# Optimization experiments

Measured on AMD Instinct MI355X. Metric: run time of the kernel, lower is better.

The kernel has to match this reference:

```python
import jax, jax.numpy as jnp
import numpy as np

B, S, F, H = 256, 512, 64, 128
ODE_STEPS = 4
MAX_DT = 1.0


def setup_inputs() -> dict:
    key = jax.random.key(0)
    ks = jax.random.split(key, 11)
    D = F + H  # concat(x_t, h) width
    xav = float(np.sqrt(6.0 / (D + H)))          # xavier_uniform for gate weights
    bsc = float(1.0 / np.sqrt(D))                # torch Linear default bias init
    x = jax.random.normal(ks[0], (B, S, F), jnp.float32)
    time_diffs = jax.random.uniform(ks[1], (B, S), jnp.float32, 0.1, 2.0)
    def w(k):
        return jax.random.uniform(k, (D, H), jnp.float32, -xav, xav)
    def b(k):
        return jax.random.uniform(k, (H,), jnp.float32, -bsc, bsc)
    return {
        "x": x, "time_diffs": time_diffs,
        "W_i": w(ks[2]), "b_i": b(ks[3]),
        "W_f": w(ks[4]), "b_f": b(ks[5]),
        "W_o": w(ks[6]), "b_o": b(ks[7]),
        "W_g": w(ks[8]), "b_g": b(ks[9]),
    }


def reference(x, time_diffs, W_i, b_i, W_f, b_f, W_o, b_o, W_g, b_g):
    def ode_func(x_t, h, c):
        comb = jnp.concatenate([x_t, h], axis=-1)  # [B, F+H]
        i = jax.nn.sigmoid(comb @ W_i + b_i)
        f = jax.nn.sigmoid(comb @ W_f + b_f)
        o = jax.nn.sigmoid(comb @ W_o + b_o)
        g = jnp.tanh(comb @ W_g + b_g)
        dc = i * g + f * c - c
        dh = o * jnp.tanh(c) - h
        return dh, dc

    def rk4_step(x_t, h, c, dt):  # dt: [B, 1]
        k1h, k1c = ode_func(x_t, h, c)
        k2h, k2c = ode_func(x_t, h + 0.5 * dt * k1h, c + 0.5 * dt * k1c)
        k3h, k3c = ode_func(x_t, h + 0.5 * dt * k2h, c + 0.5 * dt * k2c)
        k4h, k4c = ode_func(x_t, h + dt * k3h, c + dt * k3c)
        h_new = h + dt / 6.0 * (k1h + 2 * k2h + 2 * k3h + k4h)
        c_new = c + dt / 6.0 * (k1c + 2 * k2c + 2 * k3c + k4c)
        return h_new, c_new

    def time_step(carry, inp):
        h, c = carry
        x_t, dtv = inp  # x_t [B,F], dtv [B]
        sub_dt = (jnp.minimum(dtv, MAX_DT) / ODE_STEPS)[:, None]  # [B,1]
        def body(hc, _):
            hh, cc = hc
            return rk4_step(x_t, hh, cc, sub_dt), None
        (h, c), _ = jax.lax.scan(body, (h, c), None, length=ODE_STEPS)
        return (h, c), h

    h0 = jnp.zeros((x.shape[0], H), x.dtype)
    c0 = jnp.zeros((x.shape[0], H), x.dtype)
    xs = (jnp.swapaxes(x, 0, 1), jnp.swapaxes(time_diffs, 0, 1))  # [S,B,F], [S,B]
    _, hs = jax.lax.scan(time_step, (h0, c0), xs)  # [S,B,H]
    return jnp.swapaxes(hs, 0, 1)  # [B,S,H]
```

## Files before the change

kernel.cpp:

```cpp
#include <hip/hip_runtime.h>


#define B_N 256
#define S_N 512
#define F_N 64
#define H_N 128

typedef _Float16 v8h __attribute__((ext_vector_type(8)));
typedef float v4f __attribute__((ext_vector_type(4)));

#define PIN_V(x) asm("" : "+v"(x))
#define MFMA16(a, b, c) __builtin_amdgcn_mfma_f32_16x16x32_f16((a), (b), (c), 0, 0, 0)
#define SB0() __builtin_amdgcn_sched_barrier(0)
#define BAR() do { SB0(); \
                   asm volatile("s_waitcnt lgkmcnt(0)" ::: "memory"); \
                   __builtin_amdgcn_s_barrier(); SB0(); } while (0)

static __device__ __forceinline__ float sigm(float x) {
  float e = __builtin_amdgcn_exp2f(-1.442695040888963f * x);
  return __builtin_amdgcn_rcpf(1.0f + e);
}

__global__ void __launch_bounds__(512, 2) clstm_mfma6(
    const float* __restrict__ x,
    const float* __restrict__ td,
    const float* __restrict__ Wi, const float* __restrict__ bi,
    const float* __restrict__ Wf, const float* __restrict__ bff,
    const float* __restrict__ Wo, const float* __restrict__ bo,
    const float* __restrict__ Wg, const float* __restrict__ bg,
    float* __restrict__ out)
{
  const int b    = blockIdx.x;
  const int t    = threadIdx.x;
  const int wv   = t >> 6;
  const int l    = t & 63;
  const int col  = l & 15;
  const int quad = l >> 4;
  const int n    = wv * 16 + col;

  const float* Wptr[4] = {Wi, Wf, Wo, Wg};

  v8h Bh[4][4];
  v8h Bx[4][2];
#pragma unroll
  for (int g = 0; g < 4; ++g) {
    const float* W = Wptr[g];
#pragma unroll
    for (int kt = 0; kt < 4; ++kt) {
      v8h f;
#pragma unroll
      for (int j = 0; j < 8; ++j)
        f[j] = (_Float16)W[(64 + kt * 32 + quad * 8 + j) * H_N + n];
      Bh[g][kt] = f;
      PIN_V(Bh[g][kt]);
    }
#pragma unroll
    for (int kt = 0; kt < 2; ++kt) {
      v8h f;
#pragma unroll
      for (int j = 0; j < 8; ++j)
        f[j] = (_Float16)W[(kt * 32 + quad * 8 + j) * H_N + n];
      Bx[g][kt] = f;
      PIN_V(Bx[g][kt]);
    }
  }
  float bias[4];
#pragma unroll
  for (int g = 0; g < 4; ++g)
    bias[g] = (g == 0 ? bi : g == 1 ? bff : g == 2 ? bo : bg)[n];

  __shared__ alignas(16) _Float16 lds_h[2][H_N];
  __shared__ alignas(16) _Float16 lds_x[F_N];
  __shared__ float lds_td[S_N];

  lds_td[t] = td[b * S_N + t];
  if (t < 32) {
    const float* xr = x + (size_t)b * S_N * F_N;
    lds_x[2 * t]     = (_Float16)xr[2 * t];
    lds_x[2 * t + 1] = (_Float16)xr[2 * t + 1];
  }
  if (t < H_N) lds_h[0][t] = (_Float16)0.0f;

  float h0v = 0.f, c0v = 0.f;
  float h_ev = 0.f, c_ev = 0.f;
  float sum_h = 0.f, sum_c = 0.f;
  float dt = 0.f, hdt = 0.f, d6 = 0.f, d6p = 0.f;
  const v4f zf = {0.f, 0.f, 0.f, 0.f};
  v4f ci2 = zf, ci3 = zf, cf2 = zf, cf3 = zf, cg2 = zf, cg3 = zf;
  v4f xpD[4] = {zf, zf, zf, zf};
  float xn0 = 0.f, xn1 = 0.f;

  for (int s = 0; s < S_N; ++s) {
#pragma unroll
    for (int ode = 0; ode < 4; ++ode) {
#pragma unroll
      for (int st = 0; st < 4; ++st) {
        BAR();
        const _Float16* hb = lds_h[st & 1];
        v8h ah0 = *(const v8h*)(hb + quad * 8);
        v8h ah1 = *(const v8h*)(hb + 32 + quad * 8);
        v8h ah2 = *(const v8h*)(hb + 64 + quad * 8);
        v8h ah3 = *(const v8h*)(hb + 96 + quad * 8);

        if (ode == 0 && st == 0) {
          dt  = fminf(lds_td[s], 1.0f) * 0.25f;
          hdt = 0.5f * dt;
          d6  = dt * (1.0f / 6.0f);
          v8h ax0 = *(const v8h*)(lds_x + quad * 8);
          v8h ax1 = *(const v8h*)(lds_x + 32 + quad * 8);
#pragma unroll
          for (int g = 0; g < 4; ++g) {
            float bv = bias[g];
            v4f cbv = {bv, bv, bv, bv};
            v4f a = MFMA16(ax0, Bx[g][0], cbv);
            xpD[g] = MFMA16(ax1, Bx[g][1], a);
          }
          xn0 = 0.f; xn1 = 0.f;
          if (t < 32 && s + 1 < S_N) {
            const float* xr = x + (size_t)(b * S_N + s + 1) * F_N;
            xn0 = xr[2 * t]; xn1 = xr[2 * t + 1];
          }
        }
        SB0();

        float tc;
        {
          const int pr = (st == 0) ? 3 : st - 1;
          float pi = ci2[0] + ci3[0];
          float pf = cf2[0] + cf3[0];
          float pg = cg2[0] + cg3[0];
          float ai = sigm(pi);
          float af = sigm(pf);
          float ag = fmaf(2.0f, sigm(2.0f * pg), -1.0f);
          float kc = fmaf(ai, ag, (af - 1.0f) * c_ev);
          float cnx;
          if (pr == 0)      { sum_c = kc;                      cnx = fmaf(hdt, kc, c0v); }
          else if (pr == 1) { sum_c = fmaf(2.f, kc, sum_c);    cnx = fmaf(hdt, kc, c0v); }
          else if (pr == 2) { sum_c = fmaf(2.f, kc, sum_c);    cnx = fmaf(dt, kc, c0v); }
          else {
            float sc = sum_c + kc;
            float dd = (ode == 0 && st == 0) ? d6p : d6;
            c0v = fmaf(dd, sc, c0v);
            cnx = c0v;
          }
          c_ev = cnx;
          tc = fmaf(2.0f, sigm(2.0f * c_ev), -1.0f);
        }
        SB0();

        v4f co2 = MFMA16(ah0, Bh[2][0], xpD[2]);
        co2     = MFMA16(ah1, Bh[2][1], co2);
        v4f co3 = MFMA16(ah2, Bh[2][2], zf);
        co3     = MFMA16(ah3, Bh[2][3], co3);
        SB0();

        ci2 = MFMA16(ah0, Bh[0][0], xpD[0]);
        ci2 = MFMA16(ah1, Bh[0][1], ci2);
        ci3 = MFMA16(ah2, Bh[0][2], zf);
        ci3 = MFMA16(ah3, Bh[0][3], ci3);
        cf2 = MFMA16(ah0, Bh[1][0], xpD[1]);
        cf2 = MFMA16(ah1, Bh[1][1], cf2);
        cf3 = MFMA16(ah2, Bh[1][2], zf);
        cf3 = MFMA16(ah3, Bh[1][3], cf3);
        cg2 = MFMA16(ah0, Bh[3][0], xpD[3]);
        cg2 = MFMA16(ah1, Bh[3][1], cg2);
        cg3 = MFMA16(ah2, Bh[3][2], zf);
        cg3 = MFMA16(ah3, Bh[3][3], cg3);
        float po = co2[0] + co3[0];
        float ao = sigm(po);
        SB0();

        float kh = fmaf(ao, tc, -h_ev);
        float hnx;
        if (st == 0)      { sum_h = kh;                      hnx = fmaf(hdt, kh, h0v); }
        else if (st == 1) { sum_h = fmaf(2.f, kh, sum_h);    hnx = fmaf(hdt, kh, h0v); }
        else if (st == 2) { sum_h = fmaf(2.f, kh, sum_h);    hnx = fmaf(dt, kh, h0v); }
        else {
          float sh = sum_h + kh;
          h0v = fmaf(d6, sh, h0v);
          hnx = h0v;
        }
        h_ev = hnx;
        if (quad == 0) lds_h[(st & 1) ^ 1][n] = (_Float16)hnx;

        if (ode == 3 && st == 3) {
          if (t < 32 && s + 1 < S_N) {
            lds_x[2 * t]     = (_Float16)xn0;
            lds_x[2 * t + 1] = (_Float16)xn1;
          }
          if (quad == 0) out[(size_t)(b * S_N + s) * H_N + n] = h0v;
          d6p = d6;
        }
      }
    }
  }
}

extern "C" void kernel_launch(void* const* d_in, const int* in_sizes, int n_in,
                              void* d_out, int out_size, void* d_ws, size_t ws_size,
                              hipStream_t stream) {
  (void)in_sizes; (void)n_in; (void)d_ws; (void)ws_size; (void)out_size;
  clstm_mfma6<<<B_N, 512, 0, stream>>>(
      (const float*)d_in[0],
      (const float*)d_in[1],
      (const float*)d_in[2], (const float*)d_in[3],
      (const float*)d_in[4], (const float*)d_in[5],
      (const float*)d_in[6], (const float*)d_in[7],
      (const float*)d_in[8], (const float*)d_in[9],
      (float*)d_out);
}
```

Baseline: 3.585 ms.

## Defer i/f/g gate MFMAs to next stage and split o-gate chain

The i, f and g gate matrix products, which only feed the next RK stage's cell update, are moved to the start of the following stage. They now run on the saved h operands right after the barrier rather than sitting between the h update and the next barrier. The o-gate product is split into four independent MFMAs that are summed afterwards, which shortens its dependent chain. The aim is to cut latency on the serial per-stage critical path, at the cost of keeping the previous h fragments live in registers.

```diff
diff --git a/kernel.cpp b/kernel.cpp
--- a/kernel.cpp
+++ b/kernel.cpp
@@ -21,7 +21,7 @@
   return __builtin_amdgcn_rcpf(1.0f + e);
 }
 
-__global__ void __launch_bounds__(512, 2) clstm_mfma6(
+__global__ void __launch_bounds__(512, 2) clstm_mfma7(
     const float* __restrict__ x,
     const float* __restrict__ td,
     const float* __restrict__ Wi, const float* __restrict__ bi,
@@ -86,8 +86,11 @@
   float sum_h = 0.f, sum_c = 0.f;
   float dt = 0.f, hdt = 0.f, d6 = 0.f, d6p = 0.f;
   const v4f zf = {0.f, 0.f, 0.f, 0.f};
+  const v8h zh = {(_Float16)0, (_Float16)0, (_Float16)0, (_Float16)0,
+                  (_Float16)0, (_Float16)0, (_Float16)0, (_Float16)0};
   v4f ci2 = zf, ci3 = zf, cf2 = zf, cf3 = zf, cg2 = zf, cg3 = zf;
-  v4f xpD[4] = {zf, zf, zf, zf};
+  v4f xpI = zf, xpF = zf, xpO = zf, xpG = zf;
+  v8h ap0 = zh, ap1 = zh, ap2 = zh, ap3 = zh;
   float xn0 = 0.f, xn1 = 0.f;
 
   for (int s = 0; s < S_N; ++s) {
@@ -102,18 +105,43 @@
         v8h ah2 = *(const v8h*)(hb + 64 + quad * 8);
         v8h ah3 = *(const v8h*)(hb + 96 + quad * 8);
 
+        if (st != 0 || ode != 0 || s != 0) {
+          ci2 = MFMA16(ap0, Bh[0][0], xpI);
+          ci2 = MFMA16(ap1, Bh[0][1], ci2);
+          ci3 = MFMA16(ap2, Bh[0][2], zf);
+          ci3 = MFMA16(ap3, Bh[0][3], ci3);
+          cf2 = MFMA16(ap0, Bh[1][0], xpF);
+          cf2 = MFMA16(ap1, Bh[1][1], cf2);
+          cf3 = MFMA16(ap2, Bh[1][2], zf);
+          cf3 = MFMA16(ap3, Bh[1][3], cf3);
+          cg2 = MFMA16(ap0, Bh[3][0], xpG);
+          cg2 = MFMA16(ap1, Bh[3][1], cg2);
+          cg3 = MFMA16(ap2, Bh[3][2], zf);
+          cg3 = MFMA16(ap3, Bh[3][3], cg3);
+        }
+        SB0();
+
         if (ode == 0 && st == 0) {
           dt  = fminf(lds_td[s], 1.0f) * 0.25f;
           hdt = 0.5f * dt;
           d6  = dt * (1.0f / 6.0f);
           v8h ax0 = *(const v8h*)(lds_x + quad * 8);
           v8h ax1 = *(const v8h*)(lds_x + 32 + quad * 8);
-#pragma unroll
-          for (int g = 0; g < 4; ++g) {
-            float bv = bias[g];
-            v4f cbv = {bv, bv, bv, bv};
-            v4f a = MFMA16(ax0, Bx[g][0], cbv);
-            xpD[g] = MFMA16(ax1, Bx[g][1], a);
+          {
+            v4f cb = {bias[0], bias[0], bias[0], bias[0]};
+            v4f a = MFMA16(ax0, Bx[0][0], cb);  xpI = MFMA16(ax1, Bx[0][1], a);
+          }
+          {
+            v4f cb = {bias[1], bias[1], bias[1], bias[1]};
+            v4f a = MFMA16(ax0, Bx[1][0], cb);  xpF = MFMA16(ax1, Bx[1][1], a);
+          }
+          {
+            v4f cb = {bias[2], bias[2], bias[2], bias[2]};
+            v4f a = MFMA16(ax0, Bx[2][0], cb);  xpO = MFMA16(ax1, Bx[2][1], a);
+          }
+          {
+            v4f cb = {bias[3], bias[3], bias[3], bias[3]};
+            v4f a = MFMA16(ax0, Bx[3][0], cb);  xpG = MFMA16(ax1, Bx[3][1], a);
           }
           xn0 = 0.f; xn1 = 0.f;
           if (t < 32 && s + 1 < S_N) {
@@ -121,6 +149,11 @@
             xn0 = xr[2 * t]; xn1 = xr[2 * t + 1];
           }
         }
+
+        v4f co0 = MFMA16(ah0, Bh[2][0], xpO);
+        v4f co1 = MFMA16(ah1, Bh[2][1], zf);
+        v4f co2 = MFMA16(ah2, Bh[2][2], zf);
+        v4f co3 = MFMA16(ah3, Bh[2][3], zf);
         SB0();
 
         float tc;
@@ -146,30 +179,9 @@
           c_ev = cnx;
           tc = fmaf(2.0f, sigm(2.0f * c_ev), -1.0f);
         }
-        SB0();
-
-        v4f co2 = MFMA16(ah0, Bh[2][0], xpD[2]);
-        co2     = MFMA16(ah1, Bh[2][1], co2);
-        v4f co3 = MFMA16(ah2, Bh[2][2], zf);
-        co3     = MFMA16(ah3, Bh[2][3], co3);
-        SB0();
-
-        ci2 = MFMA16(ah0, Bh[0][0], xpD[0]);
-        ci2 = MFMA16(ah1, Bh[0][1], ci2);
-        ci3 = MFMA16(ah2, Bh[0][2], zf);
-        ci3 = MFMA16(ah3, Bh[0][3], ci3);
-        cf2 = MFMA16(ah0, Bh[1][0], xpD[1]);
-        cf2 = MFMA16(ah1, Bh[1][1], cf2);
-        cf3 = MFMA16(ah2, Bh[1][2], zf);
-        cf3 = MFMA16(ah3, Bh[1][3], cf3);
-        cg2 = MFMA16(ah0, Bh[3][0], xpD[3]);
-        cg2 = MFMA16(ah1, Bh[3][1], cg2);
-        cg3 = MFMA16(ah2, Bh[3][2], zf);
-        cg3 = MFMA16(ah3, Bh[3][3], cg3);
-        float po = co2[0] + co3[0];
+
+        float po = (co0[0] + co1[0]) + (co2[0] + co3[0]);
         float ao = sigm(po);
-        SB0();
-
         float kh = fmaf(ao, tc, -h_ev);
         float hnx;
         if (st == 0)      { sum_h = kh;                      hnx = fmaf(hdt, kh, h0v); }
@@ -191,6 +203,8 @@
           if (quad == 0) out[(size_t)(b * S_N + s) * H_N + n] = h0v;
           d6p = d6;
         }
+
+        ap0 = ah0; ap1 = ah1; ap2 = ah2; ap3 = ah3;
       }
     }
   }
@@ -200,7 +214,7 @@
                               void* d_out, int out_size, void* d_ws, size_t ws_size,
                               hipStream_t stream) {
   (void)in_sizes; (void)n_in; (void)d_ws; (void)ws_size; (void)out_size;
-  clstm_mfma6<<<B_N, 512, 0, stream>>>(
+  clstm_mfma7<<<B_N, 512, 0, stream>>>(
       (const float*)d_in[0],
       (const float*)d_in[1],
       (const float*)d_in[2], (const float*)d_in[3],
```

Measured after the change: 3.284 ms. 1.09x faster.
